# Kernel tuning notes

Measured on AMD Instinct MI355X. Metric: run time of the kernel, lower is better.

Reference implementation:

```python
import jax, jax.numpy as jnp
import numpy as np

L, D, DB, P, B = 33, 2048, 1024, 24, 2048
EPS = 1e-5

def _ln(x, g, b):
    # LayerNorm over last axis, eps matches torch default 1e-5
    mu = jnp.mean(x, axis=-1, keepdims=True)
    var = jnp.mean(jnp.square(x - mu), axis=-1, keepdims=True)
    return (x - mu) * jax.lax.rsqrt(var + EPS) * g + b

def setup_inputs() -> dict:
    key = jax.random.key(0)
    ks = jax.random.split(key, 8)
    s1 = 1.0 / np.sqrt(D)   # fan-in style scaling to keep activations sane
    s2 = 1.0 / np.sqrt(DB)
    sp = 1.0 / np.sqrt(P)
    return {
        "x":      jax.random.normal(ks[0], (B, L, D), jnp.float32),
        "pos_emb": jax.random.uniform(ks[1], (L, P), jnp.float32),
        "Wk":     jax.random.normal(ks[2], (P, D), jnp.float32) * sp,
        "W1":     jax.random.normal(ks[3], (L, D, DB), jnp.float32) * s1,
        "b1":     jnp.zeros((L, DB), jnp.float32),
        "ln1_g":  jnp.ones((L, DB), jnp.float32),
        "ln1_b":  jnp.zeros((L, DB), jnp.float32),
        "W2":     jax.random.normal(ks[4], (L, DB, D), jnp.float32) * s2,
        "b2":     jnp.zeros((L, D), jnp.float32),
        "ln2_g":  jnp.ones((L, D), jnp.float32),
        "ln2_b":  jnp.zeros((L, D), jnp.float32),
        "Wq1":    jax.random.normal(ks[5], (D, DB), jnp.float32) * s1,
        "bq1":    jnp.zeros((DB,), jnp.float32),
        "lnq_g":  jnp.ones((DB,), jnp.float32),
        "lnq_b":  jnp.zeros((DB,), jnp.float32),
        "Wq2":    jax.random.normal(ks[6], (DB, D), jnp.float32) * s2,
        "bq2":    jnp.zeros((D,), jnp.float32),
    }

def reference(x, pos_emb, Wk, W1, b1, ln1_g, ln1_b, W2, b2, ln2_g, ln2_b,
              Wq1, bq1, lnq_g, lnq_b, Wq2, bq2):
    # x: [B, L, D]
    z_L = x[:, -1, :]                                   # [B, D]
    keys = pos_emb @ Wk                                 # Eq.10: [L, D]
    # Eq.11 + Eq.4: per-layer value MLPs, grouped as batched GEMMs
    h = jax.nn.gelu(jnp.einsum('bld,ldk->blk', x, W1) + b1, approximate=False)
    h = _ln(h, ln1_g, ln1_b)                            # [B, L, DB]
    v = jnp.einsum('blk,lkd->bld', h, W2) + b2          # [B, L, D]
    values = _ln(v, ln2_g, ln2_b)                       # [B, L, D]
    # Eq.5: query from last layer
    hq = jax.nn.gelu(z_L @ Wq1 + bq1, approximate=False)
    hq = _ln(hq, lnq_g, lnq_b)
    q_tr = hq @ Wq2 + bq2                               # [B, D]
    query = 1.0 + jax.nn.elu(z_L + q_tr)                # [B, D]
    # Eq.7-9: single-query attention over depth + residual
    attn = jax.nn.softmax(query @ keys.T, axis=-1)      # [B, L]
    attended = jnp.einsum('bl,bld->bd', attn, values)   # [B, D]
    return z_L + attended
```

## Files before the change

kernel.cpp:

```cpp
#include <hip/hip_runtime.h>
#include <cstddef>
#include <cstdint>

#define Lc 33
#define Dc 2048
#define DBc 1024
#define Pc 24
#define Bc 2048

typedef __attribute__((ext_vector_type(4))) float f32x4;
typedef __attribute__((ext_vector_type(8))) short s16x8;
typedef __attribute__((ext_vector_type(4))) short s16x4;

__device__ __forceinline__ short bf16r(float f) {
  unsigned u = __float_as_uint(f);
  u = (u + 0x7fffu + ((u >> 16) & 1u)) >> 16;
  return (short)u;
}
__device__ __forceinline__ float bf2f(short s) {
  return __uint_as_float(((unsigned)(unsigned short)s) << 16);
}
__device__ __forceinline__ s16x8 pack8(const float* f) {
  s16x8 r;
#pragma unroll
  for (int i = 0; i < 8; ++i) r[i] = bf16r(f[i]);
  return r;
}
__device__ __forceinline__ void split8(const float* f, s16x8& hi, s16x8& lo) {
#pragma unroll
  for (int i = 0; i < 8; ++i) {
    short h = bf16r(f[i]);
    hi[i] = h;
    lo[i] = bf16r(f[i] - bf2f(h));
  }
}
__device__ __forceinline__ void gl_lds16(const void* g, void* l) {
  __builtin_amdgcn_global_load_lds(
      (const __attribute__((address_space(1))) unsigned int*)g,
      (__attribute__((address_space(3))) unsigned int*)l, 16, 0, 0);
}

__global__ __launch_bounds__(256)
void cvt_bf16_kernel(const float* __restrict__ in,
                     unsigned short* __restrict__ outp) {
  const size_t i = ((size_t)blockIdx.x * 256 + threadIdx.x) * 8;
  f32x4 a = *(const f32x4*)(in + i);
  f32x4 b = *(const f32x4*)(in + i + 4);
  float f[8] = {a[0], a[1], a[2], a[3], b[0], b[1], b[2], b[3]};
  *(s16x8*)(outp + i) = pack8(f);
}

__global__ __launch_bounds__(256)
void keys_kernel(const float* __restrict__ pe, const float* __restrict__ Wk,
                 float* __restrict__ keys) {
  const int l = blockIdx.x;
  const int d = blockIdx.y * 256 + threadIdx.x;
  float s = 0.f;
#pragma unroll
  for (int p = 0; p < Pc; ++p) s += pe[l * Pc + p] * Wk[(size_t)p * Dc + d];
  keys[(size_t)l * Dc + d] = s;
}

template <int K, int N>
__global__ __launch_bounds__(256)
void transpose_w(const float* __restrict__ W, unsigned short* __restrict__ Wt) {
  const int z = blockIdx.z;
  const int k0 = blockIdx.x * 64, n0 = blockIdx.y * 64;
  __shared__ unsigned short tile[64][66];
  const int t = threadIdx.x;
  {
    const int r = t >> 2, cq = (t & 3) * 16;
    const float* src = W + (size_t)z * K * N + (size_t)(k0 + r) * N + n0 + cq;
#pragma unroll
    for (int i = 0; i < 16; i += 4) {
      f32x4 v = *(const f32x4*)(src + i);
#pragma unroll
      for (int j = 0; j < 4; ++j)
        tile[r][cq + i + j] = (unsigned short)bf16r(v[j]);
    }
  }
  __syncthreads();
  {
    const int n = t >> 2, kc = (t & 3) * 16;
    s16x8 o0, o1;
#pragma unroll
    for (int i = 0; i < 8; ++i) {
      o0[i] = tile[kc + i][n];
      o1[i] = tile[kc + 8 + i][n];
    }
    unsigned short* dst =
        Wt + (size_t)z * N * K + (size_t)(n0 + n) * K + k0 + kc;
    *(s16x8*)dst = o0;
    *(s16x8*)(dst + 8) = o1;
  }
}

template <int K, int N, int NBM, int NBN, int GELU, int STATS>
__global__ __launch_bounds__(512, 2)
void gemm256(const unsigned short* __restrict__ A,
             const unsigned short* __restrict__ Wt,
             const float* __restrict__ bias,
             unsigned short* __restrict__ outbuf, float* __restrict__ stats) {
  constexpr int NT = K / 32;
  constexpr int nwg = 33 * NBM * NBN;
  constexpr int q = nwg >> 3, r = nwg & 7;
  const int orig = blockIdx.x;
  const int xcd = orig & 7;
  const int wgid =
      ((xcd < r) ? xcd * (q + 1) : r * (q + 1) + (xcd - r) * q) + (orig >> 3);
  const int z = wgid / (NBM * NBN);
  const int rem = wgid - z * (NBM * NBN);
  const int bm = rem / NBN;
  const int bn = rem - bm * NBN;

  const int tid = threadIdx.x, lane = tid & 63, wv = tid >> 6;
  const int wm = wv >> 2, wn = wv & 3;
  const int wr = wm * 128, wc = wn * 64;
  const int l15 = lane & 15, l4 = lane >> 4;

  __shared__ __align__(16) unsigned short Als[2][256 * 32];
  __shared__ __align__(16) unsigned short Bls[2][256 * 32];

  f32x4 acc[8][4];
#pragma unroll
  for (int m = 0; m < 8; ++m)
#pragma unroll
    for (int n = 0; n < 4; ++n) {
      acc[m][n][0] = 0.f; acc[m][n][1] = 0.f;
      acc[m][n][2] = 0.f; acc[m][n][3] = 0.f;
    }

  const int rA = lane >> 2, sA = lane & 3;
  const unsigned short* Bbase = Wt + (size_t)z * N * K;

  auto stage = [&](int buf, int kt) {
#pragma unroll
    for (int c = 0; c < 2; ++c) {
      const int rl = wv * 32 + c * 16 + rA;
      const int swz = (sA ^ (rl & 3)) * 8;
      gl_lds16(A + ((size_t)(bm * 256 + rl) * Lc + z) * K + kt * 32 + swz,
               (char*)&Als[buf][0] + wv * 2048 + c * 1024);
      gl_lds16(Bbase + (size_t)(bn * 256 + rl) * K + kt * 32 + swz,
               (char*)&Bls[buf][0] + wv * 2048 + c * 1024);
    }
  };

  stage(0, 0);
  asm volatile("s_waitcnt vmcnt(0)" ::: "memory");
  __builtin_amdgcn_s_barrier();

  for (int kt = 0; kt < NT; ++kt) {
    const int cur = kt & 1;
    if (kt + 1 < NT) stage(cur ^ 1, kt + 1);
    s16x8 bfv[4];
#pragma unroll
    for (int n = 0; n < 4; ++n) {
      const int row = wc + n * 16 + l15;
      bfv[n] = *(const s16x8*)((const char*)&Bls[cur][0] + row * 64 +
                               ((l4 ^ (row & 3)) << 4));
    }
#pragma unroll
    for (int m = 0; m < 8; ++m) {
      const int row = wr + m * 16 + l15;
      s16x8 af = *(const s16x8*)((const char*)&Als[cur][0] + row * 64 +
                                 ((l4 ^ (row & 3)) << 4));
#pragma unroll
      for (int n = 0; n < 4; ++n)
        acc[m][n] = __builtin_amdgcn_mfma_f32_16x16x32_bf16(af, bfv[n],
                                                            acc[m][n], 0, 0, 0);
    }
    asm volatile("s_waitcnt vmcnt(0)" ::: "memory");
    __builtin_amdgcn_s_barrier();
  }

  const float* biasP = bias + (size_t)z * N;
  float bsv[4];
#pragma unroll
  for (int n = 0; n < 4; ++n) bsv[n] = biasP[bn * 256 + wc + n * 16 + l15];

#pragma unroll
  for (int m = 0; m < 8; ++m) {
#pragma unroll
    for (int j = 0; j < 4; ++j) {
      const int grow = bm * 256 + wr + m * 16 + l4 * 4 + j;
      float s1 = 0.f, s2 = 0.f;
#pragma unroll
      for (int n = 0; n < 4; ++n) {
        const int col = bn * 256 + wc + n * 16 + l15;
        float v = acc[m][n][j] + bsv[n];
        if constexpr (GELU) v = 0.5f * v * (1.0f + erff(v * 0.70710678118f));
        outbuf[((size_t)grow * Lc + z) * N + col] = (unsigned short)bf16r(v);
        if constexpr (STATS) {
          s1 += v;
          s2 += v * v;
        }
      }
      if constexpr (STATS) {
#pragma unroll
        for (int o = 1; o < 16; o <<= 1) {
          s1 += __shfl_xor(s1, o);
          s2 += __shfl_xor(s2, o);
        }
        if (l15 == 0) {
          atomicAdd(&stats[((size_t)grow * Lc + z) * 2 + 0], s1);
          atomicAdd(&stats[((size_t)grow * Lc + z) * 2 + 1], s2);
        }
      }
    }
  }
}

template <int MODE, int SPLITQ>
__global__ __launch_bounds__(256, 2)
void gemm_fused(const float* __restrict__ x,
                const unsigned short* __restrict__ hbuf,
                const float* __restrict__ hqF,
                const float* __restrict__ Wmain, const float* __restrict__ Wq,
                const float* __restrict__ bmain, const float* __restrict__ bq,
                unsigned short* __restrict__ outH, float* __restrict__ outHq,
                unsigned short* __restrict__ outV, float* __restrict__ outQ) {
  constexpr int K = (MODE == 1) ? 2048 : 1024;
  constexpr int N = (MODE == 1) ? 1024 : 2048;
  constexpr int BK = 32;
  constexpr int NT = K / BK;

  const int z = blockIdx.z;
  const int bm = blockIdx.x;
  const int bn = blockIdx.y;
  const int tid = threadIdx.x;
  const int lane = tid & 63;
  const int wid = tid >> 6;
  const int wr = (wid >> 1) * 64;
  const int wc = (wid & 1) * 64;
  const int l15 = lane & 15;
  const int kb = lane >> 4;

  const float* Bp = SPLITQ ? Wq : (Wmain + (size_t)z * K * N);

  __shared__ short Als[1 + SPLITQ][128][32];
  __shared__ short Bls[1 + SPLITQ][128][32];

  const f32x4 vzero = {0.f, 0.f, 0.f, 0.f};
  f32x4 acc[4][4];
#pragma unroll
  for (int m = 0; m < 4; ++m)
#pragma unroll
    for (int n = 0; n < 4; ++n) acc[m][n] = vzero;

  const int ar = tid >> 1;
  const int ak = (tid & 1) * 16;
  const int grow = bm * 128 + ar;

  const float* ApF = nullptr;
  const unsigned short* ApH = nullptr;
  if constexpr (MODE == 1) {
    const int lsel = SPLITQ ? (Lc - 1) : z;
    ApF = x + (size_t)grow * (Lc * Dc) + (size_t)lsel * Dc + ak;
  } else if constexpr (SPLITQ == 1) {
    ApF = hqF + (size_t)grow * DBc + ak;
  } else {
    ApH = hbuf + ((size_t)grow * 33 + z) * DBc + ak;
  }

  const int bnL = tid & 127;
  const int bj = tid >> 7;
  const int c0 = ((bnL >> 1) & 3) ^ bj;
  const int kc0 = c0 * 8;
  const int kc1 = (c0 ^ 2) * 8;
  const float* Bcol = Bp + (size_t)bn * 128 + bnL;

  float aF[16];
  s16x8 aH0, aH1;
  float bF[16];

  auto loadA = [&](int kt) {
    if constexpr (MODE == 2 && SPLITQ == 0) {
      const unsigned short* p = ApH + kt * BK;
      aH0 = *(const s16x8*)p;
      aH1 = *(const s16x8*)(p + 8);
    } else {
      const float* p = ApF + kt * BK;
#pragma unroll
      for (int i = 0; i < 4; ++i) {
        f32x4 t = *(const f32x4*)(p + i * 4);
#pragma unroll
        for (int j = 0; j < 4; ++j) aF[i * 4 + j] = t[j];
      }
    }
  };
  auto loadB = [&](int kt) {
    const float* p0 = Bcol + (size_t)(kt * BK + kc0) * N;
    const float* p1 = Bcol + (size_t)(kt * BK + kc1) * N;
#pragma unroll
    for (int i = 0; i < 8; ++i) bF[i] = p0[(size_t)i * N];
#pragma unroll
    for (int i = 0; i < 8; ++i) bF[8 + i] = p1[(size_t)i * N];
  };
  auto writeLDS = [&]() {
    if constexpr (MODE == 2 && SPLITQ == 0) {
      *(s16x8*)&Als[0][ar][ak] = aH0;
      *(s16x8*)&Als[0][ar][ak + 8] = aH1;
    } else if constexpr (SPLITQ == 0) {
      *(s16x8*)&Als[0][ar][ak] = pack8(aF);
      *(s16x8*)&Als[0][ar][ak + 8] = pack8(aF + 8);
    } else {
      s16x8 h0, l0, h1, l1;
      split8(aF, h0, l0);
      split8(aF + 8, h1, l1);
      *(s16x8*)&Als[0][ar][ak] = h0;
      *(s16x8*)&Als[1][ar][ak] = l0;
      *(s16x8*)&Als[0][ar][ak + 8] = h1;
      *(s16x8*)&Als[1][ar][ak + 8] = l1;
    }
    if constexpr (SPLITQ == 0) {
      *(s16x8*)&Bls[0][bnL][kc0] = pack8(bF);
      *(s16x8*)&Bls[0][bnL][kc1] = pack8(bF + 8);
    } else {
      s16x8 h0, l0, h1, l1;
      split8(bF, h0, l0);
      split8(bF + 8, h1, l1);
      *(s16x8*)&Bls[0][bnL][kc0] = h0;
      *(s16x8*)&Bls[1][bnL][kc0] = l0;
      *(s16x8*)&Bls[0][bnL][kc1] = h1;
      *(s16x8*)&Bls[1][bnL][kc1] = l1;
    }
  };

  loadA(0);
  loadB(0);
  for (int kt = 0; kt < NT; ++kt) {
    __syncthreads();
    writeLDS();
    if (kt + 1 < NT) {
      loadA(kt + 1);
      loadB(kt + 1);
    }
    __syncthreads();
    s16x8 af[4], bfv[4];
#pragma unroll
    for (int m = 0; m < 4; ++m)
      af[m] = *(const s16x8*)&Als[0][wr + m * 16 + l15][kb * 8];
#pragma unroll
    for (int n = 0; n < 4; ++n)
      bfv[n] = *(const s16x8*)&Bls[0][wc + n * 16 + l15][kb * 8];
    if constexpr (SPLITQ == 1) {
      s16x8 afl[4], bfl[4];
#pragma unroll
      for (int m = 0; m < 4; ++m)
        afl[m] = *(const s16x8*)&Als[1][wr + m * 16 + l15][kb * 8];
#pragma unroll
      for (int n = 0; n < 4; ++n)
        bfl[n] = *(const s16x8*)&Bls[1][wc + n * 16 + l15][kb * 8];
#pragma unroll
      for (int m = 0; m < 4; ++m)
#pragma unroll
        for (int n = 0; n < 4; ++n) {
          acc[m][n] = __builtin_amdgcn_mfma_f32_16x16x32_bf16(
              af[m], bfv[n], acc[m][n], 0, 0, 0);
          acc[m][n] = __builtin_amdgcn_mfma_f32_16x16x32_bf16(
              af[m], bfl[n], acc[m][n], 0, 0, 0);
          acc[m][n] = __builtin_amdgcn_mfma_f32_16x16x32_bf16(
              afl[m], bfv[n], acc[m][n], 0, 0, 0);
        }
    } else {
#pragma unroll
      for (int m = 0; m < 4; ++m)
#pragma unroll
        for (int n = 0; n < 4; ++n)
          acc[m][n] = __builtin_amdgcn_mfma_f32_16x16x32_bf16(
              af[m], bfv[n], acc[m][n], 0, 0, 0);
    }
  }

  const float* biasP = SPLITQ ? bq : (bmain + (size_t)z * N);
#pragma unroll
  for (int m = 0; m < 4; ++m) {
    const int r0 = bm * 128 + wr + m * 16 + kb * 4;
#pragma unroll
    for (int n = 0; n < 4; ++n) {
      const int col = bn * 128 + wc + n * 16 + l15;
      const float bs = biasP[col];
#pragma unroll
      for (int j = 0; j < 4; ++j) {
        const int r = r0 + j;
        const float v = acc[m][n][j] + bs;
        if constexpr (MODE == 1 && SPLITQ == 0) {
          const float g = 0.5f * v * (1.0f + erff(v * 0.70710678118f));
          outH[((size_t)r * 33 + z) * DBc + col] = (unsigned short)bf16r(g);
        } else if constexpr (MODE == 1 && SPLITQ == 1) {
          const float g = 0.5f * v * (1.0f + erff(v * 0.70710678118f));
          outHq[(size_t)r * DBc + col] = g;
        } else if constexpr (MODE == 2 && SPLITQ == 0) {
          outV[((size_t)r * 33 + z) * Dc + col] = (unsigned short)bf16r(v);
        } else {
          const float zl =
              x[(size_t)r * (Lc * Dc) + (size_t)(Lc - 1) * Dc + col];
          const float t = zl + v;
          outQ[(size_t)r * Dc + col] = (t > 0.f) ? (1.f + t) : __expf(t);
        }
      }
    }
  }
}

template <int W>
__global__ __launch_bounds__(256)
void ln_kernel(unsigned short* __restrict__ buf, const float* __restrict__ gmain,
               const float* __restrict__ bmain) {
  constexpr int E = W / 256;
  const int z = blockIdx.x;
  const int b = blockIdx.y;
  const int tid = threadIdx.x;
  unsigned short* row = buf + ((size_t)b * 33 + z) * W;
  float v[E];
  if constexpr (E == 4) {
    s16x4 t = *(const s16x4*)(row + tid * 4);
#pragma unroll
    for (int i = 0; i < 4; ++i) v[i] = bf2f(t[i]);
  } else {
    s16x8 t = *(const s16x8*)(row + tid * 8);
#pragma unroll
    for (int i = 0; i < 8; ++i) v[i] = bf2f(t[i]);
  }
  float s = 0.f, s2 = 0.f;
#pragma unroll
  for (int i = 0; i < E; ++i) {
    s += v[i];
    s2 += v[i] * v[i];
  }
#pragma unroll
  for (int o = 32; o > 0; o >>= 1) {
    s += __shfl_xor(s, o);
    s2 += __shfl_xor(s2, o);
  }
  __shared__ float red[2][4];
  const int w = tid >> 6;
  if ((tid & 63) == 0) {
    red[0][w] = s;
    red[1][w] = s2;
  }
  __syncthreads();
  s = red[0][0] + red[0][1] + red[0][2] + red[0][3];
  s2 = red[1][0] + red[1][1] + red[1][2] + red[1][3];
  const float mu = s * (1.0f / W);
  const float var = s2 * (1.0f / W) - mu * mu;
  const float rstd = rsqrtf(var + 1e-5f);
  const float* G = gmain + (size_t)z * W;
  const float* Bt = bmain + (size_t)z * W;
  if constexpr (E == 4) {
    f32x4 gv = *(const f32x4*)(G + tid * 4);
    f32x4 bv = *(const f32x4*)(Bt + tid * 4);
    s16x4 o;
#pragma unroll
    for (int i = 0; i < 4; ++i)
      o[i] = bf16r((v[i] - mu) * rstd * gv[i] + bv[i]);
    *(s16x4*)(row + tid * 4) = o;
  } else {
    f32x4 g0 = *(const f32x4*)(G + tid * 8);
    f32x4 g1 = *(const f32x4*)(G + tid * 8 + 4);
    f32x4 b0 = *(const f32x4*)(Bt + tid * 8);
    f32x4 b1 = *(const f32x4*)(Bt + tid * 8 + 4);
    s16x8 o;
#pragma unroll
    for (int i = 0; i < 4; ++i) {
      o[i] = bf16r((v[i] - mu) * rstd * g0[i] + b0[i]);
      o[i + 4] = bf16r((v[i + 4] - mu) * rstd * g1[i] + b1[i]);
    }
    *(s16x8*)(row + tid * 8) = o;
  }
}

__global__ __launch_bounds__(256)
void stats_kernel(const unsigned short* __restrict__ vals,
                  float* __restrict__ stats) {
  const int z = blockIdx.x;
  const int b = blockIdx.y;
  const int tid = threadIdx.x;
  const unsigned short* row = vals + ((size_t)b * 33 + z) * Dc;
  s16x8 t = *(const s16x8*)(row + tid * 8);
  float s = 0.f, s2 = 0.f;
#pragma unroll
  for (int i = 0; i < 8; ++i) {
    float v = bf2f(t[i]);
    s += v;
    s2 += v * v;
  }
#pragma unroll
  for (int o = 32; o > 0; o >>= 1) {
    s += __shfl_xor(s, o);
    s2 += __shfl_xor(s2, o);
  }
  __shared__ float red[2][4];
  const int w = tid >> 6;
  if ((tid & 63) == 0) {
    red[0][w] = s;
    red[1][w] = s2;
  }
  __syncthreads();
  if (tid == 0) {
    stats[((size_t)b * 33 + z) * 2 + 0] =
        red[0][0] + red[0][1] + red[0][2] + red[0][3];
    stats[((size_t)b * 33 + z) * 2 + 1] =
        red[1][0] + red[1][1] + red[1][2] + red[1][3];
  }
}

__global__ __launch_bounds__(256)
void ln_f32_kernel(float* __restrict__ buf, const float* __restrict__ g,
                   const float* __restrict__ bb) {
  const int r = blockIdx.x;
  const int tid = threadIdx.x;
  float* row = buf + (size_t)r * DBc;
  f32x4 v = *(const f32x4*)(row + tid * 4);
  float s = 0.f, s2 = 0.f;
#pragma unroll
  for (int i = 0; i < 4; ++i) {
    s += v[i];
    s2 += v[i] * v[i];
  }
#pragma unroll
  for (int o = 32; o > 0; o >>= 1) {
    s += __shfl_xor(s, o);
    s2 += __shfl_xor(s2, o);
  }
  __shared__ float red[2][4];
  const int w = tid >> 6;
  if ((tid & 63) == 0) {
    red[0][w] = s;
    red[1][w] = s2;
  }
  __syncthreads();
  s = red[0][0] + red[0][1] + red[0][2] + red[0][3];
  s2 = red[1][0] + red[1][1] + red[1][2] + red[1][3];
  const float mu = s * (1.0f / DBc);
  const float var = s2 * (1.0f / DBc) - mu * mu;
  const float rstd = rsqrtf(var + 1e-5f);
  f32x4 gv = *(const f32x4*)(g + tid * 4);
  f32x4 bv = *(const f32x4*)(bb + tid * 4);
  f32x4 o;
#pragma unroll
  for (int i = 0; i < 4; ++i) o[i] = (v[i] - mu) * rstd * gv[i] + bv[i];
  *(f32x4*)(row + tid * 4) = o;
}

__global__ __launch_bounds__(256)
void attn_kernel(const float* __restrict__ x, const float* __restrict__ query,
                 const float* __restrict__ keys,
                 const unsigned short* __restrict__ vals,
                 const float* __restrict__ stats, const float* __restrict__ g2,
                 const float* __restrict__ b2ln, float* __restrict__ out) {
  const int b = blockIdx.x;
  const int tid = threadIdx.x;
  const int d0 = tid * 8;

  float qv[8];
  {
    f32x4 t0 = *(const f32x4*)(query + (size_t)b * Dc + d0);
    f32x4 t1 = *(const f32x4*)(query + (size_t)b * Dc + d0 + 4);
#pragma unroll
    for (int i = 0; i < 4; ++i) {
      qv[i] = t0[i];
      qv[i + 4] = t1[i];
    }
  }
  float s[33];
#pragma unroll
  for (int l = 0; l < 33; ++l) {
    const float* kp = keys + (size_t)l * Dc + d0;
    f32x4 k0 = *(const f32x4*)kp;
    f32x4 k1 = *(const f32x4*)(kp + 4);
    float t = 0.f;
#pragma unroll
    for (int i = 0; i < 4; ++i) t += qv[i] * k0[i] + qv[i + 4] * k1[i];
    s[l] = t;
  }
#pragma unroll
  for (int l = 0; l < 33; ++l) {
    float v = s[l];
#pragma unroll
    for (int o = 32; o > 0; o >>= 1) v += __shfl_xor(v, o);
    s[l] = v;
  }
  __shared__ float sred[4][33];
  __shared__ float sl[33];
  const int w = tid >> 6;
  if ((tid & 63) == 0) {
#pragma unroll
    for (int l = 0; l < 33; ++l) sred[w][l] = s[l];
  }
  __syncthreads();
  if (tid < 33)
    sl[tid] = sred[0][tid] + sred[1][tid] + sred[2][tid] + sred[3][tid];
  __syncthreads();

  float m = -1e30f;
#pragma unroll
  for (int l = 0; l < 33; ++l) m = fmaxf(m, sl[l]);
  float p[33];
  float sum = 0.f;
#pragma unroll
  for (int l = 0; l < 33; ++l) {
    p[l] = __expf(sl[l] - m);
    sum += p[l];
  }
  const float inv = 1.0f / sum;

  float acc8[8];
  {
    const float* zl = x + (size_t)b * (Lc * Dc) + (size_t)(Lc - 1) * Dc + d0;
    f32x4 z0 = *(const f32x4*)zl;
    f32x4 z1 = *(const f32x4*)(zl + 4);
#pragma unroll
    for (int i = 0; i < 4; ++i) {
      acc8[i] = z0[i];
      acc8[i + 4] = z1[i];
    }
  }
  const unsigned short* vb = vals + (size_t)b * 33 * Dc + d0;
#pragma unroll
  for (int l = 0; l < 33; ++l) {
    const float st0 = stats[((size_t)b * 33 + l) * 2 + 0];
    const float st1 = stats[((size_t)b * 33 + l) * 2 + 1];
    const float mu = st0 * (1.0f / Dc);
    const float var = st1 * (1.0f / Dc) - mu * mu;
    const float rstd = rsqrtf(var + 1e-5f);
    const float a = p[l] * inv;
    s16x8 vv = *(const s16x8*)(vb + (size_t)l * Dc);
    const float* gp = g2 + (size_t)l * Dc + d0;
    const float* bp = b2ln + (size_t)l * Dc + d0;
    f32x4 g0 = *(const f32x4*)gp, g1 = *(const f32x4*)(gp + 4);
    f32x4 b0 = *(const f32x4*)bp, b1 = *(const f32x4*)(bp + 4);
#pragma unroll
    for (int i = 0; i < 4; ++i) {
      acc8[i] += a * ((bf2f(vv[i]) - mu) * rstd * g0[i] + b0[i]);
      acc8[i + 4] += a * ((bf2f(vv[i + 4]) - mu) * rstd * g1[i] + b1[i]);
    }
  }
  f32x4 o0, o1;
#pragma unroll
  for (int i = 0; i < 4; ++i) {
    o0[i] = acc8[i];
    o1[i] = acc8[i + 4];
  }
  *(f32x4*)(out + (size_t)b * Dc + d0) = o0;
  *(f32x4*)(out + (size_t)b * Dc + d0 + 4) = o1;
}

extern "C" void kernel_launch(void* const* d_in, const int* in_sizes, int n_in,
                              void* d_out, int out_size, void* d_ws,
                              size_t ws_size, hipStream_t stream) {
  const float* x = (const float*)d_in[0];
  const float* pe = (const float*)d_in[1];
  const float* Wk = (const float*)d_in[2];
  const float* W1 = (const float*)d_in[3];
  const float* b1 = (const float*)d_in[4];
  const float* ln1g = (const float*)d_in[5];
  const float* ln1b = (const float*)d_in[6];
  const float* W2 = (const float*)d_in[7];
  const float* b2 = (const float*)d_in[8];
  const float* ln2g = (const float*)d_in[9];
  const float* ln2b = (const float*)d_in[10];
  const float* Wq1 = (const float*)d_in[11];
  const float* bq1 = (const float*)d_in[12];
  const float* lnqg = (const float*)d_in[13];
  const float* lnqb = (const float*)d_in[14];
  const float* Wq2 = (const float*)d_in[15];
  const float* bq2 = (const float*)d_in[16];
  float* out = (float*)d_out;
  char* ws = (char*)d_ws;

  float* keysP = (float*)(ws);
  float* queryP = (float*)(ws + 270336);
  float* hqP = (float*)(ws + 17047552);
  float* statsP = (float*)(ws + 25436160);
  unsigned short* hP = (unsigned short*)(ws + 25976832);
  unsigned short* xbfP = (unsigned short*)(ws + 164388864);
  unsigned short* valsP = (unsigned short*)(ws + 164388864);
  unsigned short* W1tP = (unsigned short*)(ws + 441212928);
  unsigned short* W2tP = (unsigned short*)(ws + 441212928);

  const bool fast = (ws_size >= 579624960ull);

  keys_kernel<<<dim3(33, 8), 256, 0, stream>>>(pe, Wk, keysP);

  gemm_fused<1, 1><<<dim3(16, 8, 1), 256, 0, stream>>>(
      x, nullptr, nullptr, nullptr, Wq1, nullptr, bq1, nullptr, hqP, nullptr,
      nullptr);

  if (fast) {
    cvt_bf16_kernel<<<dim3(67584), 256, 0, stream>>>(x, xbfP);
    transpose_w<2048, 1024><<<dim3(32, 16, 33), 256, 0, stream>>>(W1, W1tP);
    gemm256<2048, 1024, 8, 4, 1, 0><<<dim3(33 * 8 * 4), 512, 0, stream>>>(
        xbfP, W1tP, b1, hP, nullptr);
  } else {
    gemm_fused<1, 0><<<dim3(16, 8, 33), 256, 0, stream>>>(
        x, nullptr, nullptr, W1, nullptr, b1, nullptr, hP, nullptr, nullptr,
        nullptr);
  }

  ln_kernel<1024><<<dim3(33, 2048), 256, 0, stream>>>(hP, ln1g, ln1b);

  ln_f32_kernel<<<dim3(2048), 256, 0, stream>>>(hqP, lnqg, lnqb);

  hipMemsetAsync(statsP, 0, 2048 * 33 * 2 * sizeof(float), stream);

  if (fast) {
    transpose_w<1024, 2048><<<dim3(16, 32, 33), 256, 0, stream>>>(W2, W2tP);
    gemm256<1024, 2048, 8, 8, 0, 1><<<dim3(33 * 8 * 8), 512, 0, stream>>>(
        hP, W2tP, b2, valsP, statsP);
  } else {
    gemm_fused<2, 0><<<dim3(16, 16, 33), 256, 0, stream>>>(
        x, hP, nullptr, W2, nullptr, b2, nullptr, nullptr, nullptr, valsP,
        nullptr);
    stats_kernel<<<dim3(33, 2048), 256, 0, stream>>>(valsP, statsP);
  }

  gemm_fused<2, 1><<<dim3(16, 16, 1), 256, 0, stream>>>(
      x, nullptr, hqP, nullptr, Wq2, nullptr, bq2, nullptr, nullptr, nullptr,
      queryP);

  attn_kernel<<<dim3(2048), 256, 0, stream>>>(x, queryP, keysP, valsP, statsP,
                                              ln2g, ln2b, out);
}
```

Before: 1.910 ms.

## Replace 256x256 batched GEMM with 8-phase pipelined kernel using 128KB dynamic LDS

Rewrites the main batched bf16 GEMM so that each iteration covers two 64-wide K tiles, split into eight phases. Each phase interleaves LDS fragment reads, a half-tile global-to-LDS prefetch, and a 16-MFMA cluster raised to high priority with s_setprio. Partial vmcnt waits and barriers keep loads in flight across phases, so memory latency is meant to overlap with MFMA work. It requires 128KB of dynamic shared memory, which could reduce occupancy; if that attribute cannot be set, a new 128x128 two-phase GEMM plus a separate stats kernel is used instead.

```diff
diff --git a/kernel.cpp b/kernel.cpp
--- a/kernel.cpp
+++ b/kernel.cpp
@@ -39,6 +39,9 @@
       (const __attribute__((address_space(1))) unsigned int*)g,
       (__attribute__((address_space(3))) unsigned int*)l, 16, 0, 0);
 }
+
+#define BARw() __builtin_amdgcn_s_barrier()
+#define VM4() asm volatile("s_waitcnt vmcnt(4)" ::: "memory")
 
 __global__ __launch_bounds__(256)
 void cvt_bf16_kernel(const float* __restrict__ in,
@@ -95,13 +98,17 @@
   }
 }
 
-template <int K, int N, int NBM, int NBN, int GELU, int STATS>
+template <int K, int N, int NBN, int GELU, int STATS>
 __global__ __launch_bounds__(512, 2)
-void gemm256(const unsigned short* __restrict__ A,
+void gemm8ph(const unsigned short* __restrict__ A,
              const unsigned short* __restrict__ Wt,
              const float* __restrict__ bias,
              unsigned short* __restrict__ outbuf, float* __restrict__ stats) {
-  constexpr int NT = K / 32;
+  constexpr int NT = K / 64;
+  constexpr int NIT = NT / 2;
+  constexpr int NBM = 8;
+  extern __shared__ __align__(16) char smem[];
+
   constexpr int nwg = 33 * NBM * NBN;
   constexpr int q = nwg >> 3, r = nwg & 7;
   const int orig = blockIdx.x;
@@ -110,17 +117,13 @@
       ((xcd < r) ? xcd * (q + 1) : r * (q + 1) + (xcd - r) * q) + (orig >> 3);
   const int z = wgid / (NBM * NBN);
   const int rem = wgid - z * (NBM * NBN);
-  const int bm = rem / NBN;
-  const int bn = rem - bm * NBN;
+  const int bm = rem / NBN, bn = rem - bm * NBN;
 
   const int tid = threadIdx.x, lane = tid & 63, wv = tid >> 6;
   const int wm = wv >> 2, wn = wv & 3;
   const int wr = wm * 128, wc = wn * 64;
   const int l15 = lane & 15, l4 = lane >> 4;
 
-  __shared__ __align__(16) unsigned short Als[2][256 * 32];
-  __shared__ __align__(16) unsigned short Bls[2][256 * 32];
-
   f32x4 acc[8][4];
 #pragma unroll
   for (int m = 0; m < 8; ++m)
@@ -130,48 +133,101 @@
       acc[m][n][2] = 0.f; acc[m][n][3] = 0.f;
     }
 
-  const int rA = lane >> 2, sA = lane & 3;
-  const unsigned short* Bbase = Wt + (size_t)z * N * K;
-
-  auto stage = [&](int buf, int kt) {
+  const int srow = lane >> 2, sslot = lane & 3;
+  const int sswz = (sslot ^ (srow & 3)) * 8;
+
+  const unsigned short* aRow[2];
+  const unsigned short* bRow[2];
+  {
+    const unsigned short* Bbase = Wt + (size_t)z * N * K;
 #pragma unroll
     for (int c = 0; c < 2; ++c) {
-      const int rl = wv * 32 + c * 16 + rA;
-      const int swz = (sA ^ (rl & 3)) * 8;
-      gl_lds16(A + ((size_t)(bm * 256 + rl) * Lc + z) * K + kt * 32 + swz,
-               (char*)&Als[buf][0] + wv * 2048 + c * 1024);
-      gl_lds16(Bbase + (size_t)(bn * 256 + rl) * K + kt * 32 + swz,
-               (char*)&Bls[buf][0] + wv * 2048 + c * 1024);
-    }
+      const int gr = (wv * 2 + c) * 16 + srow;
+      aRow[c] = A + (size_t)(bm * 256 + gr) * ((size_t)Lc * K) +
+                (size_t)z * K + sswz;
+      bRow[c] = Bbase + (size_t)(bn * 256 + gr) * K + sswz;
+    }
+  }
+
+  auto STAGE_A = [&](int t, int kh) {
+    char* dst = smem + (t & 1) * 65536 + kh * 16384 + wv * 2048;
+    const int ko = t * 64 + kh * 32;
+#pragma unroll
+    for (int c = 0; c < 2; ++c) gl_lds16(aRow[c] + ko, dst + c * 1024);
   };
-
-  stage(0, 0);
-  asm volatile("s_waitcnt vmcnt(0)" ::: "memory");
-  __builtin_amdgcn_s_barrier();
-
-  for (int kt = 0; kt < NT; ++kt) {
-    const int cur = kt & 1;
-    if (kt + 1 < NT) stage(cur ^ 1, kt + 1);
-    s16x8 bfv[4];
+  auto STAGE_B = [&](int t, int kh) {
+    char* dst = smem + (t & 1) * 65536 + 32768 + kh * 16384 + wv * 2048;
+    const int ko = t * 64 + kh * 32;
+#pragma unroll
+    for (int c = 0; c < 2; ++c) gl_lds16(bRow[c] + ko, dst + c * 1024);
+  };
+  s16x8 afr[4], bfr[4];
+  auto LDA = [&](int d, int kk, int mh) {
+#pragma unroll
+    for (int m = 0; m < 4; ++m) {
+      const int row = wr + (mh * 4 + m) * 16 + l15;
+      afr[m] = *(const s16x8*)(smem + d * 65536 + kk * 16384 + row * 64 +
+                               ((l4 ^ (row & 3)) << 4));
+    }
+  };
+  auto LDB = [&](int d, int kk) {
 #pragma unroll
     for (int n = 0; n < 4; ++n) {
       const int row = wc + n * 16 + l15;
-      bfv[n] = *(const s16x8*)((const char*)&Bls[cur][0] + row * 64 +
-                               ((l4 ^ (row & 3)) << 4));
-    }
-#pragma unroll
-    for (int m = 0; m < 8; ++m) {
-      const int row = wr + m * 16 + l15;
-      s16x8 af = *(const s16x8*)((const char*)&Als[cur][0] + row * 64 +
-                                 ((l4 ^ (row & 3)) << 4));
-#pragma unroll
-      for (int n = 0; n < 4; ++n)
-        acc[m][n] = __builtin_amdgcn_mfma_f32_16x16x32_bf16(af, bfv[n],
-                                                            acc[m][n], 0, 0, 0);
-    }
-    asm volatile("s_waitcnt vmcnt(0)" ::: "memory");
-    __builtin_amdgcn_s_barrier();
-  }
+      bfr[n] = *(const s16x8*)(smem + d * 65536 + 32768 + kk * 16384 +
+                               row * 64 + ((l4 ^ (row & 3)) << 4));
+    }
+  };
+
+#define MFMA16(MH)                                                          \
+  {                                                                         \
+    __builtin_amdgcn_s_setprio(1);                                          \
+    _Pragma("unroll") for (int m_ = 0; m_ < 4; ++m_) {                      \
+      _Pragma("unroll") for (int n_ = 0; n_ < 4; ++n_) {                    \
+        acc[(MH) * 4 + m_][n_] = __builtin_amdgcn_mfma_f32_16x16x32_bf16(   \
+            afr[m_], bfr[n_], acc[(MH) * 4 + m_][n_], 0, 0, 0);             \
+      }                                                                     \
+    }                                                                       \
+    __builtin_amdgcn_s_setprio(0);                                          \
+  }
+
+  STAGE_A(0, 0); STAGE_B(0, 0); STAGE_A(0, 1); STAGE_B(0, 1);
+  STAGE_A(1, 0); STAGE_B(1, 0);
+  VM4();
+  BARw();
+
+  for (int i = 0; i < NIT; ++i) {
+    const int t0 = 2 * i, t1 = 2 * i + 1;
+    LDA(0, 0, 0); LDB(0, 0);
+    STAGE_A(t1, 1);
+    BARw(); MFMA16(0); BARw();
+    LDA(0, 0, 1);
+    STAGE_B(t1, 1);
+    BARw(); MFMA16(1); BARw();
+    LDA(0, 1, 0); LDB(0, 1);
+    if (t0 + 2 < NT) STAGE_A(t0 + 2, 0);
+    BARw(); MFMA16(0); BARw();
+    LDA(0, 1, 1);
+    if (t0 + 2 < NT) STAGE_B(t0 + 2, 0);
+    BARw(); MFMA16(1);
+    VM4();
+    BARw();
+    LDA(1, 0, 0); LDB(1, 0);
+    if (t0 + 2 < NT) STAGE_A(t0 + 2, 1);
+    BARw(); MFMA16(0); BARw();
+    LDA(1, 0, 1);
+    if (t0 + 2 < NT) STAGE_B(t0 + 2, 1);
+    BARw(); MFMA16(1); BARw();
+    LDA(1, 1, 0); LDB(1, 1);
+    if (t0 + 3 < NT) STAGE_A(t0 + 3, 0);
+    BARw(); MFMA16(0); BARw();
+    LDA(1, 1, 1);
+    if (t0 + 3 < NT) STAGE_B(t0 + 3, 0);
+    BARw(); MFMA16(1);
+    VM4();
+    BARw();
+  }
+#undef MFMA16
 
   const float* biasP = bias + (size_t)z * N;
   float bsv[4];
@@ -205,6 +261,99 @@
           atomicAdd(&stats[((size_t)grow * Lc + z) * 2 + 0], s1);
           atomicAdd(&stats[((size_t)grow * Lc + z) * 2 + 1], s2);
         }
+      }
+    }
+  }
+}
+
+template <int K, int N, int GELU>
+__global__ __launch_bounds__(256, 2)
+void gemm2ph(const unsigned short* __restrict__ A,
+             const unsigned short* __restrict__ Wt,
+             const float* __restrict__ bias,
+             unsigned short* __restrict__ outbuf) {
+  constexpr int NT = K / 64;
+  const int z = blockIdx.z, bm = blockIdx.x, bn = blockIdx.y;
+  const int tid = threadIdx.x, lane = tid & 63, w = tid >> 6;
+  const int wr = (w >> 1) * 64, wc = (w & 1) * 64;
+  const int l15 = lane & 15, kb = lane >> 4;
+
+  __shared__ __align__(16) unsigned short Als[2][128 * 64];
+  __shared__ __align__(16) unsigned short Bls[2][128 * 64];
+
+  f32x4 acc[4][4];
+#pragma unroll
+  for (int m = 0; m < 4; ++m)
+#pragma unroll
+    for (int n = 0; n < 4; ++n) {
+      acc[m][n][0] = 0.f; acc[m][n][1] = 0.f;
+      acc[m][n][2] = 0.f; acc[m][n][3] = 0.f;
+    }
+
+  const int rl8 = lane >> 3, sl = lane & 7;
+  const int swzE = ((sl ^ rl8) << 3);
+  const unsigned short* Bbase = Wt + (size_t)z * N * K;
+
+  auto stage = [&](int buf, int kt) {
+#pragma unroll
+    for (int j = 0; j < 4; ++j) {
+      const int rloc = w * 32 + j * 8 + rl8;
+      gl_lds16(A + ((size_t)(bm * 128 + rloc) * Lc + z) * K + kt * 64 + swzE,
+               (char*)&Als[buf][0] + w * 4096 + j * 1024);
+      gl_lds16(Bbase + (size_t)(bn * 128 + rloc) * K + kt * 64 + swzE,
+               (char*)&Bls[buf][0] + w * 4096 + j * 1024);
+    }
+  };
+
+  stage(0, 0);
+  asm volatile("s_waitcnt vmcnt(0)" ::: "memory");
+  __builtin_amdgcn_s_barrier();
+
+  for (int kt = 0; kt < NT; ++kt) {
+    const int cur = kt & 1;
+    if (kt + 1 < NT) stage(cur ^ 1, kt + 1);
+#pragma unroll
+    for (int kk = 0; kk < 2; ++kk) {
+      s16x8 af[4], bfv[4];
+#pragma unroll
+      for (int m = 0; m < 4; ++m) {
+        const int row = wr + m * 16 + l15;
+        const int slot = kk * 4 + kb;
+        af[m] = *(const s16x8*)((const char*)&Als[cur][0] + row * 128 +
+                                ((slot ^ (row & 7)) << 4));
+      }
+#pragma unroll
+      for (int n = 0; n < 4; ++n) {
+        const int row = wc + n * 16 + l15;
+        const int slot = kk * 4 + kb;
+        bfv[n] = *(const s16x8*)((const char*)&Bls[cur][0] + row * 128 +
+                                 ((slot ^ (row & 7)) << 4));
+      }
+#pragma unroll
+      for (int m = 0; m < 4; ++m)
+#pragma unroll
+        for (int n = 0; n < 4; ++n)
+          acc[m][n] = __builtin_amdgcn_mfma_f32_16x16x32_bf16(
+              af[m], bfv[n], acc[m][n], 0, 0, 0);
+    }
+    asm volatile("s_waitcnt vmcnt(0)" ::: "memory");
+    __builtin_amdgcn_s_barrier();
+  }
+
+  const float* biasP = bias + (size_t)z * N;
+#pragma unroll
+  for (int m = 0; m < 4; ++m) {
+    const int r0 = bm * 128 + wr + m * 16 + kb * 4;
+#pragma unroll
+    for (int n = 0; n < 4; ++n) {
+      const int col = bn * 128 + wc + n * 16 + l15;
+      const float bs = biasP[col];
+#pragma unroll
+      for (int j = 0; j < 4; ++j) {
+        const int r = r0 + j;
+        float v = acc[m][n][j] + bs;
+        if constexpr (GELU) v = 0.5f * v * (1.0f + erff(v * 0.70710678118f));
+        outbuf[((size_t)r * Lc + z) * N + col] = (unsigned short)bf16r(v);
       }
     }
   }
@@ -680,6 +829,17 @@
   unsigned short* W2tP = (unsigned short*)(ws + 441212928);
 
   const bool fast = (ws_size >= 579624960ull);
+  bool use8 = fast;
+  if (fast) {
+    if (hipFuncSetAttribute(
+            reinterpret_cast<const void*>(&gemm8ph<2048, 1024, 4, 1, 0>),
+            hipFuncAttributeMaxDynamicSharedMemorySize, 131072) != hipSuccess)
+      use8 = false;
+    if (hipFuncSetAttribute(
+            reinterpret_cast<const void*>(&gemm8ph<1024, 2048, 8, 0, 1>),
+            hipFuncAttributeMaxDynamicSharedMemorySize, 131072) != hipSuccess)
+      use8 = false;
+  }
 
   keys_kernel<<<dim3(33, 8), 256, 0, stream>>>(pe, Wk, keysP);
 
@@ -690,8 +850,13 @@
   if (fast) {
     cvt_bf16_kernel<<<dim3(67584), 256, 0, stream>>>(x, xbfP);
     transpose_w<2048, 1024><<<dim3(32, 16, 33), 256, 0, stream>>>(W1, W1tP);
-    gemm256<2048, 1024, 8, 4, 1, 0><<<dim3(33 * 8 * 4), 512, 0, stream>>>(
-        xbfP, W1tP, b1, hP, nullptr);
+    if (use8) {
+      gemm8ph<2048, 1024, 4, 1, 0><<<dim3(33 * 8 * 4), 512, 131072, stream>>>(
+          xbfP, W1tP, b1, hP, nullptr);
+    } else {
+      gemm2ph<2048, 1024, 1><<<dim3(16, 8, 33), 256, 0, stream>>>(xbfP, W1tP,
+                                                                  b1, hP);
+    }
   } else {
     gemm_fused<1, 0><<<dim3(16, 8, 33), 256, 0, stream>>>(
         x, nullptr, nullptr, W1, nullptr, b1, nullptr, hP, nullptr, nullptr,
@@ -706,8 +871,14 @@
 
   if (fast) {
     transpose_w<1024, 2048><<<dim3(16, 32, 33), 256, 0, stream>>>(W2, W2tP);
-    gemm256<1024, 2048, 8, 8, 0, 1><<<dim3(33 * 8 * 8), 512, 0, stream>>>(
-        hP, W2tP, b2, valsP, statsP);
+    if (use8) {
+      gemm8ph<1024, 2048, 8, 0, 1><<<dim3(33 * 8 * 8), 512, 131072, stream>>>(
+          hP, W2tP, b2, valsP, statsP);
+    } else {
+      gemm2ph<1024, 2048, 0><<<dim3(16, 16, 33), 256, 0, stream>>>(hP, W2tP,
+                                                                   b2, valsP);
+      stats_kernel<<<dim3(33, 2048), 256, 0, stream>>>(valsP, statsP);
+    }
   } else {
     gemm_fused<2, 0><<<dim3(16, 16, 33), 256, 0, stream>>>(
         x, hP, nullptr, W2, nullptr, b2, nullptr, nullptr, nullptr, valsP,
```

Measured after the change: 1.625 ms. 14.9% less time.
